# Kernel optimization log

Hardware: AMD Instinct MI355X
Metric: run time of the kernel (lower is better)

## Reference

```python
import jax, jax.numpy as jnp
import numpy as np

D, N = 256, 16384
EPS = 1e-8


def setup_inputs() -> dict:
    key = jax.random.key(0)
    weight = jax.random.normal(key, (D, N), dtype=jnp.float32)
    return {"weight": weight, "loss_weight": jnp.float32(1.0)}


def reference(weight, loss_weight):
    # Original: for each column i, target = weight.data[:, i] (detached, broadcast to [d, n]);
    #   a_j = cos(weight[:, j], target_i); loss_i = log(sum_j exp(a_j - 1)); total = lw * sum_i loss_i / n.
    # Vectorized: G[i, j] = sg(w_hat_i) . w_hat_j  (single GEMM on the column-normalized matrix).
    d, n = weight.shape
    norms = jnp.linalg.norm(weight, axis=0, keepdims=True)            # [1, n]
    wn = weight / jnp.maximum(norms, EPS)                              # column-normalized, eps-clamped like F.cosine_similarity
    wn_sg = jax.lax.stop_gradient(wn)                                  # target used weight.data (detached)
    G = jnp.einsum('di,dj->ij', wn_sg, wn)                             # [n, n] cosine-similarity Gram
    loss = jnp.sum(jnp.log(jnp.sum(jnp.exp(G - 1.0), axis=1)))         # row-wise exp/sum/log, summed over rows
    return loss_weight * loss / n
```

## Files before the change

kernel.cpp:

```cpp
#include <hip/hip_runtime.h>
#include <hip/hip_bf16.h>

#define NCOLS 16384
#define DDIM  256
#define SUBT  32
#define CHUNK 43
#define GRID  768
#define SQRT_L2E 1.2011224087864498f

typedef __attribute__((ext_vector_type(8))) short bf16x8;
typedef __attribute__((ext_vector_type(4))) float f32x4;
typedef __attribute__((ext_vector_type(4))) int   i32x4;

typedef __attribute__((address_space(1))) const unsigned int gu32;
typedef __attribute__((address_space(3))) unsigned int       lu32;

static __device__ __forceinline__ ushort f2bf_rne(float f) {
    unsigned u = __builtin_bit_cast(unsigned, f);
    unsigned r = (u + 0x7fffu + ((u >> 16) & 1u)) >> 16;
    return (ushort)r;
}

__global__ __launch_bounds__(256)
void k_norm(const float* __restrict__ W, ushort* __restrict__ wnT,
            float* __restrict__ S) {
    __shared__ float red[8][32];
    __shared__ float scale_s[32];
    const int tid = threadIdx.x;
    const int il = tid & 31, st = tid >> 5;
    const int col = blockIdx.x * 32 + il;
    float v[32];
    float p = 0.f;
    #pragma unroll
    for (int e = 0; e < 32; ++e) {
        v[e] = W[(size_t)(st * 32 + e) * NCOLS + col];
        p = fmaf(v[e], v[e], p);
    }
    red[st][il] = p;
    __syncthreads();
    if (tid < 32) {
        float n = 0.f;
        #pragma unroll
        for (int q = 0; q < 8; ++q) n += red[q][tid];
        scale_s[tid] = SQRT_L2E / fmaxf(sqrtf(n), 1e-8f);
        S[blockIdx.x * 32 + tid] = 0.f;
    }
    __syncthreads();
    const float sc = scale_s[il];
    #pragma unroll
    for (int g = 0; g < 4; ++g) {
        union { ushort us[8]; i32x4 w4; } pk;
        #pragma unroll
        for (int e2 = 0; e2 < 8; ++e2) pk.us[e2] = f2bf_rne(v[g * 8 + e2] * sc);
        *reinterpret_cast<i32x4*>(&wnT[(size_t)col * DDIM + st * 32 + g * 8]) = pk.w4;
    }
}

__global__ __launch_bounds__(256, 3)
void k_gram(const ushort* __restrict__ wnT, float* __restrict__ S) {
    __shared__ ushort Bs[2][SUBT * DDIM];
    __shared__ float colLDS[2][4][256];

    const int bid = blockIdx.x;
    const int sr  = bid / 12, cch = bid - sr * 12;
    const int rowA = sr, rowB = 127 - sr;
    const int La = 512 - 4 * rowA;
    const int p0 = cch * CHUNK;

    const int tid  = threadIdx.x;
    const int lane = tid & 63, wave = tid >> 6;
    const int l15  = lane & 15;
    const int kq16 = ((lane >> 4) & 3) * 16;
    const int xorm = (lane & 7) << 4;

    bf16x8 afrag[2][8];
    float rowsum[2][4];

    auto load_a = [&](int rowt) {
        const int i0 = rowt * 128;
        #pragma unroll
        for (int s = 0; s < 2; ++s) {
            const ushort* arow = wnT +
                (size_t)(i0 + wave * 32 + s * 16 + l15) * DDIM + (kq16 >> 1);
            #pragma unroll
            for (int kk = 0; kk < 8; ++kk)
                afrag[s][kk] = *reinterpret_cast<const bf16x8*>(arow + kk * 32);
        }
    };
    auto zero_rows = [&]() {
        #pragma unroll
        for (int s = 0; s < 2; ++s)
            #pragma unroll
            for (int r = 0; r < 4; ++r) rowsum[s][r] = 0.f;
    };
    auto flush_rows = [&](int i0) {
        #pragma unroll
        for (int s = 0; s < 2; ++s)
            #pragma unroll
            for (int r = 0; r < 4; ++r) {
                float v = rowsum[s][r];
                v += __shfl_xor(v, 1, 64);
                v += __shfl_xor(v, 2, 64);
                v += __shfl_xor(v, 4, 64);
                v += __shfl_xor(v, 8, 64);
                if (l15 == 0)
                    atomicAdd(&S[i0 + wave * 32 + s * 16 + (lane >> 4) * 4 + r], v);
            }
    };
    auto stage = [&](int b, int j0) {
        #pragma unroll
        for (int qq = 0; qq < 4; ++qq) {
            const int r0 = wave * 8 + qq * 2;
            const int rl = r0 + (lane >> 5);
            const int sb = ((lane & 31) * 16) ^ ((rl & 7) << 4);
            const ushort* g = wnT + (size_t)(j0 + rl) * DDIM + (sb >> 1);
            char* l = (char*)&Bs[b][0] + (r0 << 9);
            __builtin_amdgcn_global_load_lds((gu32*)g, (lu32*)l, 16, 0, 0);
        }
    };
    auto flush_group = [&](int g) {
        const int slot = tid >> 5, cc = tid & 31;
        const int p = p0 + g * 8 + slot;
        if (p < p0 + CHUNK) {
            const bool inA = (p < La);
            const int prow = inA ? rowA : rowB;
            const int pk   = inA ? p : p - La;
            if (pk >= 4) {
                const int o = slot * 32 + cc;
                float v = colLDS[g & 1][0][o] + colLDS[g & 1][1][o] +
                          colLDS[g & 1][2][o] + colLDS[g & 1][3][o];
                atomicAdd(&S[prow * 128 + pk * 32 + cc], v);
            }
        }
    };

    int crow = (p0 < La) ? rowA : rowB;
    load_a(crow);
    zero_rows();
    {
        const int pk0 = (p0 < La) ? p0 : p0 - La;
        stage(0, crow * 128 + pk0 * 32);
    }
    __syncthreads();

    for (int q = 0; q < CHUNK; ++q) {
        const int p = p0 + q;
        if (q > 0 && p == La) {
            flush_rows(rowA * 128);
            zero_rows();
            load_a(rowB);
            crow = rowB;
        }
        if (q < CHUNK - 1) {
            const int pn = p + 1;
            const bool nA = (pn < La);
            const int nrow = nA ? rowA : rowB;
            const int nk   = nA ? pn : pn - La;
            stage((q + 1) & 1, nrow * 128 + nk * 32);
        }
        if (q >= 8 && (q & 7) == 0) flush_group((q >> 3) - 1);

        const char* bufbase = (const char*)&Bs[q & 1][0];
        const int slot = q & 7, cbuf = (q >> 3) & 1;
        float colp0 = 0.f, colp1 = 0.f;
        #pragma unroll
        for (int jj = 0; jj < 2; ++jj) {
            const char* brow = bufbase + ((jj * 16 + l15) << 9);
            bf16x8 b[8];
            #pragma unroll
            for (int kk = 0; kk < 8; ++kk)
                b[kk] = *reinterpret_cast<const bf16x8*>(
                    brow + ((kk * 64 + kq16) ^ xorm));
            __builtin_amdgcn_s_setprio(1);
            #pragma unroll
            for (int s = 0; s < 2; ++s) {
                f32x4 acc = {0.f, 0.f, 0.f, 0.f};
                #pragma unroll
                for (int kk = 0; kk < 8; ++kk)
                    acc = __builtin_amdgcn_mfma_f32_16x16x32_bf16(
                        afrag[s][kk], b[kk], acc, 0, 0, 0);
                __builtin_amdgcn_s_setprio(0);
                #pragma unroll
                for (int r = 0; r < 4; ++r) {
                    float e = __builtin_amdgcn_exp2f(acc[r]);
                    rowsum[s][r] += e;
                    if (jj == 0) colp0 += e; else colp1 += e;
                }
                __builtin_amdgcn_s_setprio(1);
            }
            __builtin_amdgcn_s_setprio(0);
        }
        {
            float v = colp0;
            v += __shfl_xor(v, 16, 64);
            v += __shfl_xor(v, 32, 64);
            if (lane < 16) colLDS[cbuf][wave][slot * 32 + l15] = v;
            float w = colp1;
            w += __shfl_xor(w, 16, 64);
            w += __shfl_xor(w, 32, 64);
            if (lane < 16) colLDS[cbuf][wave][slot * 32 + 16 + l15] = w;
        }
        __syncthreads();
    }
    flush_group((CHUNK - 1) >> 3);
    flush_rows(crow * 128);
}

__global__ __launch_bounds__(1024)
void k_final(const float* __restrict__ S, const float* __restrict__ lw,
             float* __restrict__ out) {
    float a = 0.f;
    for (int i = threadIdx.x; i < NCOLS; i += 1024)
        a += __builtin_amdgcn_logf(S[i]);
    #pragma unroll
    for (int m2 = 1; m2 < 64; m2 <<= 1) a += __shfl_xor(a, m2, 64);
    __shared__ float red[16];
    if ((threadIdx.x & 63) == 0) red[threadIdx.x >> 6] = a;
    __syncthreads();
    if (threadIdx.x == 0) {
        float tot = 0.f;
        #pragma unroll
        for (int q2 = 0; q2 < 16; ++q2) tot += red[q2];
        out[0] = lw[0] * (tot * 0.6931471805599453f - (float)NCOLS) / (float)NCOLS;
    }
}

extern "C" void kernel_launch(void* const* d_in, const int* in_sizes, int n_in,
                              void* d_out, int out_size, void* d_ws, size_t ws_size,
                              hipStream_t stream) {
    const float* W  = (const float*)d_in[0];
    const float* lw = (const float*)d_in[1];
    float* out = (float*)d_out;

    ushort* wnT = (ushort*)d_ws;
    float*  S   = (float*)((char*)d_ws + (size_t)NCOLS * DDIM * 2);

    k_norm <<<NCOLS / 32, 256, 0, stream>>>(W, wnT, S);
    k_gram <<<GRID, 256, 0, stream>>>(wnT, S);
    k_final<<<1, 1024, 0, stream>>>(S, lw, out);
}
```

Baseline: 158.0 us.

## Triple-buffer B tiles with vmcnt waits and accumulate column sums in LDS

Replaces the double-buffered B staging with a three-deep ring. Each step waits on vmcnt(4) plus a raw barrier instead of a full __syncthreads, so loads run two tiles ahead. Per-tile column partials are now accumulated with LDS atomics into a per-block buffer and flushed to global once at the end, instead of in periodic group flushes. The grid drops from 768 to 512 blocks with an XCD-aware block-to-work mapping, at the cost of more LDS per block, which may lower occupancy.

```diff
diff --git a/kernel.cpp b/kernel.cpp
--- a/kernel.cpp
+++ b/kernel.cpp
@@ -3,9 +3,6 @@
 
 #define NCOLS 16384
 #define DDIM  256
-#define SUBT  32
-#define CHUNK 43
-#define GRID  768
 #define SQRT_L2E 1.2011224087864498f
 
 typedef __attribute__((ext_vector_type(8))) short bf16x8;
@@ -58,20 +55,26 @@
 
 __global__ __launch_bounds__(256, 3)
 void k_gram(const ushort* __restrict__ wnT, float* __restrict__ S) {
-    __shared__ ushort Bs[2][SUBT * DDIM];
-    __shared__ float colLDS[2][4][256];
+    __shared__ ushort Bs[3][32 * DDIM];
+    __shared__ float colAcc[65 * 32];
 
     const int bid = blockIdx.x;
-    const int sr  = bid / 12, cch = bid - sr * 12;
+    const int x   = bid & 7;
+    const int idx = bid >> 3;
+    const int sr  = x + 8 * (idx >> 3);
+    const int cch = idx & 7;
     const int rowA = sr, rowB = 127 - sr;
-    const int La = 512 - 4 * rowA;
-    const int p0 = cch * CHUNK;
+    const int La  = 512 - 4 * rowA;
+    const int cnt = 64 + (cch < 4 ? 1 : 0);
+    const int p0  = cch * 64 + (cch < 4 ? cch : 4);
 
     const int tid  = threadIdx.x;
     const int lane = tid & 63, wave = tid >> 6;
     const int l15  = lane & 15;
     const int kq16 = ((lane >> 4) & 3) * 16;
     const int xorm = (lane & 7) << 4;
+
+    for (int o = tid; o < 65 * 32; o += 256) colAcc[o] = 0.f;
 
     bf16x8 afrag[2][8];
     float rowsum[2][4];
@@ -107,7 +110,11 @@
                     atomicAdd(&S[i0 + wave * 32 + s * 16 + (lane >> 4) * 4 + r], v);
             }
     };
-    auto stage = [&](int b, int j0) {
+    auto stage = [&](int b, int p) {
+        const bool inA = (p < La);
+        const int prow = inA ? rowA : rowB;
+        const int pk   = inA ? p : p - La;
+        const int j0   = prow * 128 + pk * 32;
         #pragma unroll
         for (int qq = 0; qq < 4; ++qq) {
             const int r0 = wave * 8 + qq * 2;
@@ -118,50 +125,26 @@
             __builtin_amdgcn_global_load_lds((gu32*)g, (lu32*)l, 16, 0, 0);
         }
     };
-    auto flush_group = [&](int g) {
-        const int slot = tid >> 5, cc = tid & 31;
-        const int p = p0 + g * 8 + slot;
-        if (p < p0 + CHUNK) {
-            const bool inA = (p < La);
-            const int prow = inA ? rowA : rowB;
-            const int pk   = inA ? p : p - La;
-            if (pk >= 4) {
-                const int o = slot * 32 + cc;
-                float v = colLDS[g & 1][0][o] + colLDS[g & 1][1][o] +
-                          colLDS[g & 1][2][o] + colLDS[g & 1][3][o];
-                atomicAdd(&S[prow * 128 + pk * 32 + cc], v);
-            }
-        }
-    };
 
     int crow = (p0 < La) ? rowA : rowB;
     load_a(crow);
     zero_rows();
-    {
-        const int pk0 = (p0 < La) ? p0 : p0 - La;
-        stage(0, crow * 128 + pk0 * 32);
-    }
-    __syncthreads();
-
-    for (int q = 0; q < CHUNK; ++q) {
+    stage(0, p0);
+    stage(1, p0 + 1);
+
+    for (int q = 0; q < cnt; ++q) {
         const int p = p0 + q;
+        asm volatile("s_waitcnt vmcnt(4)" ::: "memory");
+        __builtin_amdgcn_s_barrier();
         if (q > 0 && p == La) {
             flush_rows(rowA * 128);
             zero_rows();
             load_a(rowB);
             crow = rowB;
         }
-        if (q < CHUNK - 1) {
-            const int pn = p + 1;
-            const bool nA = (pn < La);
-            const int nrow = nA ? rowA : rowB;
-            const int nk   = nA ? pn : pn - La;
-            stage((q + 1) & 1, nrow * 128 + nk * 32);
-        }
-        if (q >= 8 && (q & 7) == 0) flush_group((q >> 3) - 1);
-
-        const char* bufbase = (const char*)&Bs[q & 1][0];
-        const int slot = q & 7, cbuf = (q >> 3) & 1;
+        if (q + 2 < cnt) stage((q + 2) % 3, p + 2);
+
+        const char* bufbase = (const char*)&Bs[q % 3][0];
         float colp0 = 0.f, colp1 = 0.f;
         #pragma unroll
         for (int jj = 0; jj < 2; ++jj) {
@@ -194,16 +177,23 @@
             float v = colp0;
             v += __shfl_xor(v, 16, 64);
             v += __shfl_xor(v, 32, 64);
-            if (lane < 16) colLDS[cbuf][wave][slot * 32 + l15] = v;
+            if (lane < 16) atomicAdd(&colAcc[q * 32 + l15], v);
             float w = colp1;
             w += __shfl_xor(w, 16, 64);
             w += __shfl_xor(w, 32, 64);
-            if (lane < 16) colLDS[cbuf][wave][slot * 32 + 16 + l15] = w;
-        }
-        __syncthreads();
-    }
-    flush_group((CHUNK - 1) >> 3);
+            if (lane < 16) atomicAdd(&colAcc[q * 32 + 16 + l15], w);
+        }
+    }
     flush_rows(crow * 128);
+    __syncthreads();
+    for (int o = tid; o < cnt * 32; o += 256) {
+        const int qq = o >> 5, cc = o & 31;
+        const int p = p0 + qq;
+        const bool inA = (p < La);
+        const int prow = inA ? rowA : rowB;
+        const int pk   = inA ? p : p - La;
+        if (pk >= 4) atomicAdd(&S[prow * 128 + pk * 32 + cc], colAcc[o]);
+    }
 }
 
 __global__ __launch_bounds__(1024)
@@ -236,6 +226,6 @@
     float*  S   = (float*)((char*)d_ws + (size_t)NCOLS * DDIM * 2);
 
     k_norm <<<NCOLS / 32, 256, 0, stream>>>(W, wnT, S);
-    k_gram <<<GRID, 256, 0, stream>>>(wnT, S);
+    k_gram <<<512, 256, 0, stream>>>(wnT, S);
     k_final<<<1, 1024, 0, stream>>>(S, lw, out);
 }
```

After: 172.9 us. 9.5% more time.
